# Kernel tuning notes

Measured on AMD Instinct MI355X. Metric: run time of the kernel, lower is better.

Reference implementation:

```python
import jax, jax.numpy as jnp
import numpy as np

LN_EPS = 1e-5

def split_feature(x, ns):
    # [b,h,w,c] -> [b*ns*ns, h/ns, w/ns, c] (channel_last window split)
    b, h, w, c = x.shape
    return (x.reshape(b, ns, h // ns, ns, w // ns, c)
             .transpose(0, 1, 3, 2, 4, 5)
             .reshape(b * ns * ns, h // ns, w // ns, c))

def merge_splits(x, ns):
    bn, hs, ws, c = x.shape
    b = bn // (ns * ns)
    return (x.reshape(b, ns, ns, hs, ws, c)
             .transpose(0, 1, 3, 2, 4, 5)
             .reshape(b, hs * ns, ws * ns, c))

def layer_norm(x, g, b):
    mu = jnp.mean(x, axis=-1, keepdims=True)
    var = jnp.mean(jnp.square(x - mu), axis=-1, keepdims=True)
    return (x - mu) * jax.lax.rsqrt(var + LN_EPS) * g + b

def swin_attention(q, k, v, ns, h, w, attn_mask):
    # single-head shifted-window attention, q/k/v: [b, h*w, c]
    b, _, c = q.shape
    q = q.reshape(b, h, w, c)
    k = k.reshape(b, h, w, c)
    v = v.reshape(b, h, w, c)
    sh, sw = (h // ns) // 2, (w // ns) // 2
    q = jnp.roll(q, (-sh, -sw), axis=(1, 2))
    k = jnp.roll(k, (-sh, -sw), axis=(1, 2))
    v = jnp.roll(v, (-sh, -sw), axis=(1, 2))
    qw = split_feature(q, ns).reshape(b * ns * ns, -1, c)
    kw = split_feature(k, ns).reshape(b * ns * ns, -1, c)
    vw = split_feature(v, ns).reshape(b * ns * ns, -1, c)
    scale = 1.0 / jnp.sqrt(jnp.asarray(c, qw.dtype))
    scores = jnp.einsum('blc,bsc->bls', qw, kw) * scale
    scores = scores + jnp.tile(attn_mask, (b, 1, 1))  # mask: [ns*ns, Lw, Lw]
    attn = jax.nn.softmax(scores, axis=-1)
    out = jnp.einsum('bls,bsc->blc', attn, vw)
    out = merge_splits(out.reshape(b * ns * ns, h // ns, w // ns, c), ns)
    out = jnp.roll(out, (sh, sw), axis=(1, 2))
    return out.reshape(b, h * w, c)

def transformer_layer(source, target, mask, Wq, Wk, Wv, Wm,
                      ln1_g, ln1_b, W1, W2, ln2_g, ln2_b, h, w, ns):
    q = source @ Wq.T
    k = target @ Wk.T
    v = target @ Wv.T
    msg = swin_attention(q, k, v, ns, h, w, mask)
    msg = layer_norm(msg @ Wm.T, ln1_g, ln1_b)
    hid = jnp.concatenate([source, msg], axis=-1) @ W1.T
    msg = jax.nn.gelu(hid, approximate=False) @ W2.T
    msg = layer_norm(msg, ln2_g, ln2_b)
    return source + msg

def setup_inputs() -> dict:
    key = jax.random.key(0)
    ks = jax.random.split(key, 12)
    b, h, w, d = 8, 64, 64, 256
    ns = 2
    Lw = (h // ns) * (w // ns)
    s = 0.02
    return {
        'source': jax.random.normal(ks[0], (b, h * w, d), jnp.float32),
        'target': jax.random.normal(ks[1], (b, h * w, d), jnp.float32),
        'shifted_window_attn_mask': jax.random.normal(ks[2], (ns * ns, Lw, Lw), jnp.float32),
        'Wq': jax.random.normal(ks[3], (d, d), jnp.float32) * s,
        'Wk': jax.random.normal(ks[4], (d, d), jnp.float32) * s,
        'Wv': jax.random.normal(ks[5], (d, d), jnp.float32) * s,
        'Wm': jax.random.normal(ks[6], (d, d), jnp.float32) * s,
        'ln1_g': jnp.ones((d,), jnp.float32),
        'ln1_b': jnp.zeros((d,), jnp.float32),
        'W1': jax.random.normal(ks[7], (2 * d * 4, 2 * d), jnp.float32) * s,
        'W2': jax.random.normal(ks[8], (d, 2 * d * 4), jnp.float32) * s,
        'ln2_g': jnp.ones((d,), jnp.float32),
        'ln2_b': jnp.zeros((d,), jnp.float32),
        'height': h,
        'width': w,
        'attn_num_splits': ns,
    }

def reference(source, target, shifted_window_attn_mask, Wq, Wk, Wv, Wm,
              ln1_g, ln1_b, W1, W2, ln2_g, ln2_b, height, width, attn_num_splits):
    return transformer_layer(source, target, shifted_window_attn_mask,
                             Wq, Wk, Wv, Wm, ln1_g, ln1_b, W1, W2,
                             ln2_g, ln2_b, height, width, attn_num_splits)
```

## Files before the change

### kernel.cpp

```cpp
#include <hip/hip_runtime.h>
#include <hip/hip_bf16.h>


using bf16 = __hip_bfloat16;
typedef __attribute__((ext_vector_type(8))) short short8;
typedef __attribute__((ext_vector_type(4))) float f32x4;

__device__ __forceinline__ float bf2f(unsigned short b) {
    return __uint_as_float(((unsigned)b) << 16);
}
__device__ __forceinline__ unsigned short f2bf(float f) {
    unsigned u = __float_as_uint(f);
    unsigned r = (u + 0x7FFFu + ((u >> 16) & 1u)) >> 16;
    return (unsigned short)r;
}
__device__ __forceinline__ void cp16(const void* g, void* l) {
    __builtin_amdgcn_global_load_lds((const __attribute__((address_space(1))) void*)g,
                                     (__attribute__((address_space(3))) void*)l,
                                     16, 0, 0);
}
__device__ __forceinline__ float fast_gelu(float v) {
    const float z = v * (0.7978845608028654f + 0.0356774081f * v * v);
    const float t = 1.f - 2.f / (__expf(2.f * z) + 1.f);
    return 0.5f * v * (1.f + t);
}

constexpr int MODE_PLAIN = 0;
constexpr int MODE_QKV   = 1;
constexpr int MODE_GELU  = 3;

template<int MODE, bool CONCAT>
__global__ __launch_bounds__(256)
void gemm_bt(const bf16* __restrict__ A, const bf16* __restrict__ A2,
             const bf16* __restrict__ Bm, void* __restrict__ C,
             int K, int ldc, long sAz, long sBz, int nlog)
{
    __shared__ __align__(16) bf16 As[128 * 64];
    __shared__ __align__(16) bf16 Bs[128 * 64];

    const int z = blockIdx.z;
    A  += (long)z * sAz;
    Bm += (long)z * sBz;

    const int tid  = threadIdx.x;
    const int wave = tid >> 6, lane = tid & 63;
    const int wm = wave >> 1, wn = wave & 1;
    const int quad = lane >> 4, lrow = lane & 15;

    int m0, n0;
    if (nlog >= 0) {
        const int lin = blockIdx.x;
        const int xcd = lin & 7;
        const int s   = lin >> 3;
        const int ni  = s & ((1 << nlog) - 1);
        const int mi  = ((s >> nlog) << 3) | xcd;
        m0 = mi * 128; n0 = ni * 128;
    } else {
        m0 = blockIdx.x * 128; n0 = blockIdx.y * 128;
    }

    f32x4 acc[4][4];
#pragma unroll
    for (int i = 0; i < 4; i++)
#pragma unroll
        for (int j = 0; j < 4; j++) acc[i][j] = (f32x4){0.f, 0.f, 0.f, 0.f};

    for (int k0 = 0; k0 < K; k0 += 64) {
#pragma unroll
        for (int i = 0; i < 4; ++i) {
            const int li  = i * 256 + tid;
            const int row = li >> 3, g = li & 7;
            const int sgo = ((g ^ row) & 7) << 3;
            const bf16* ga;
            if (CONCAT) {
                ga = (k0 < 256) ? (A  + (long)(m0 + row) * 256 + k0 + sgo)
                                : (A2 + (long)(m0 + row) * 256 + (k0 - 256) + sgo);
            } else {
                ga = A + (long)(m0 + row) * K + k0 + sgo;
            }
            cp16(ga, As + (li << 3));
            const bf16* gb = Bm + (long)(n0 + row) * K + k0 + sgo;
            cp16(gb, Bs + (li << 3));
        }
        __syncthreads();

#pragma unroll
        for (int s = 0; s < 2; ++s) {
            short8 af[4], bfv[4];
#pragma unroll
            for (int i = 0; i < 4; i++) {
                const int ra = wm * 64 + i * 16 + lrow;
                const int rb = wn * 64 + i * 16 + lrow;
                const int h  = (s << 2) + quad;
                af[i]  = *(const short8*)(As + ra * 64 + (((h ^ ra) & 7) << 3));
                bfv[i] = *(const short8*)(Bs + rb * 64 + (((h ^ rb) & 7) << 3));
            }
#pragma unroll
            for (int i = 0; i < 4; i++)
#pragma unroll
                for (int j = 0; j < 4; j++)
                    acc[i][j] = __builtin_amdgcn_mfma_f32_16x16x32_bf16(
                        af[i], bfv[j], acc[i][j], 0, 0, 0);
        }
        __syncthreads();
    }

    unsigned short* outb = (unsigned short*)C;
    if (MODE == MODE_QKV) {
#pragma unroll
        for (int i = 0; i < 4; i++)
#pragma unroll
            for (int j = 0; j < 4; j++)
#pragma unroll
                for (int r = 0; r < 4; r++) {
                    const int gm = m0 + wm * 64 + i * 16 + quad * 4 + r;
                    const int gn = n0 + wn * 64 + j * 16 + lrow;
                    const int batch = gm >> 12, pos = gm & 4095;
                    const int ii = pos >> 6, jj = pos & 63;
                    const int ri = (ii + 48) & 63, rj = (jj + 48) & 63;
                    const long prow =
                        ((long)((batch << 2) + ((ri >> 5) << 1) + (rj >> 5)) << 10)
                        + ((ri & 31) << 5) + (rj & 31);
                    outb[prow * 256 + gn] = f2bf(acc[i][j][r]);
                }
    } else {
#pragma unroll
        for (int i = 0; i < 4; i++)
#pragma unroll
            for (int j = 0; j < 4; j++)
#pragma unroll
                for (int r = 0; r < 4; r++) {
                    const int gm = m0 + wm * 64 + i * 16 + quad * 4 + r;
                    const int gn = n0 + wn * 64 + j * 16 + lrow;
                    float v = acc[i][j][r];
                    if (MODE == MODE_GELU) v = fast_gelu(v);
                    outb[(long)gm * ldc + gn] = f2bf(v);
                }
    }
}

__device__ __forceinline__ void stage_kv(const bf16* __restrict__ Kp,
                                         const bf16* __restrict__ Vp,
                                         bf16* ksl, bf16* vsl,
                                         int kb0, int tid)
{
#pragma unroll
    for (int i = 0; i < 4; ++i) {
        const int li = i * 256 + tid;
        const int key = li >> 5, g = li & 31;
        const int sg = (g & 24) | ((g ^ key) & 7);
        cp16(Kp + (long)(kb0 + key) * 256 + (sg << 3), ksl + (li << 3));
    }
#pragma unroll
    for (int i = 0; i < 4; ++i) {
        const int li = i * 256 + tid;
        const int ch = li >> 2, g = li & 3;
        cp16(Vp + ((long)ch << 10) + kb0 + (g << 3), vsl + (li << 3));
    }
}

__global__ __launch_bounds__(256)
void flash_attn(const bf16* __restrict__ Q, const bf16* __restrict__ Kw,
                const bf16* __restrict__ VT, const bf16* __restrict__ mask16,
                bf16* __restrict__ msg)
{
    __shared__ __align__(16) bf16 Ks[2 * 32 * 256];
    __shared__ __align__(16) bf16 Vs[2 * 256 * 32];
    __shared__ __align__(16) unsigned short Pm[4][16 * 32];

    const int f   = blockIdx.x;
    const int win = (f & 7) | ((f >> 7) << 3);
    const int qb  = (f >> 3) & 15;
    const int m0  = qb << 6;

    const bf16* Qp = Q  + ((long)win << 18);
    const bf16* Kp = Kw + ((long)win << 18);
    const bf16* Vp = VT + ((long)win << 18);
    const unsigned short* mk =
        (const unsigned short*)mask16 + ((long)(win & 3) << 20);

    const int tid = threadIdx.x;
    const int wave = tid >> 6, lane = tid & 63;
    const int quad = lane >> 4, lrow = lane & 15;
    unsigned short* Pw = Pm[wave];

    short8 qf[8];
    {
        const bf16* qr = Qp + (long)(m0 + (wave << 4) + lrow) * 256 + quad * 8;
#pragma unroll
        for (int kc = 0; kc < 8; ++kc) qf[kc] = *(const short8*)(qr + kc * 32);
    }

    f32x4 o[16];
#pragma unroll
    for (int nf = 0; nf < 16; ++nf) o[nf] = (f32x4){0.f, 0.f, 0.f, 0.f};
    float l_lane[4] = {0.f, 0.f, 0.f, 0.f};

    stage_kv(Kp, Vp, Ks, Vs, 0, tid);

    const int mrow = m0 + (wave << 4) + (quad << 2);

    for (int kt = 0; kt < 32; ++kt) {
        const int cur = kt & 1;
        const int kb0 = kt << 5;

        unsigned short mreg[2][4];
#pragma unroll
        for (int r = 0; r < 4; ++r)
#pragma unroll
            for (int nf = 0; nf < 2; ++nf)
                mreg[nf][r] = mk[((long)(mrow + r) << 10)
                                 | (kb0 + (nf << 4) + lrow)];

        const int nxt = ((kt + 1) & 31) << 5;
        stage_kv(Kp, Vp, Ks + (cur ^ 1) * 8192, Vs + (cur ^ 1) * 8192, nxt, tid);

        asm volatile("s_waitcnt vmcnt(16)" ::: "memory");
        __builtin_amdgcn_sched_barrier(0);
        __builtin_amdgcn_s_barrier();
        __builtin_amdgcn_sched_barrier(0);

        f32x4 s[2];
        s[0] = (f32x4){0.f, 0.f, 0.f, 0.f};
        s[1] = (f32x4){0.f, 0.f, 0.f, 0.f};
        const bf16* kbase = Ks + cur * 8192;
        __builtin_amdgcn_s_setprio(1);
#pragma unroll
        for (int nf = 0; nf < 2; ++nf) {
            const int key = (nf << 4) + lrow;
            short8 kb[8];
#pragma unroll
            for (int kc = 0; kc < 8; ++kc) {
                const int g = (kc << 2) + quad;
                const int sg = (g & 24) | ((g ^ key) & 7);
                kb[kc] = *(const short8*)(kbase + (key << 8) + (sg << 3));
            }
#pragma unroll
            for (int kc = 0; kc < 8; ++kc)
                s[nf] = __builtin_amdgcn_mfma_f32_16x16x32_bf16(
                    qf[kc], kb[kc], s[nf], 0, 0, 0);
        }
        __builtin_amdgcn_s_setprio(0);

#pragma unroll
        for (int r = 0; r < 4; ++r) {
            const int prow = (quad << 2) + r;
#pragma unroll
            for (int nf = 0; nf < 2; ++nf) {
                const float e = __expf(s[nf][r] * 0.0625f + bf2f(mreg[nf][r]));
                l_lane[r] += e;
                Pw[(prow << 5) + (nf << 4) + lrow] = f2bf(e);
            }
        }
        asm volatile("s_waitcnt lgkmcnt(0)" ::: "memory");
        __builtin_amdgcn_sched_barrier(0);

        const short8 af = *(const short8*)((const unsigned short*)Pw
                                           + (lrow << 5) + (quad << 3));
        const bf16* vbase = Vs + cur * 8192;
        __builtin_amdgcn_s_setprio(1);
#pragma unroll
        for (int nf = 0; nf < 16; ++nf) {
            const int vc = (nf << 4) + lrow;
            const short8 bfv = *(const short8*)(vbase + (vc << 5) + (quad << 3));
            o[nf] = __builtin_amdgcn_mfma_f32_16x16x32_bf16(af, bfv, o[nf], 0, 0, 0);
        }
        __builtin_amdgcn_s_setprio(0);

        __builtin_amdgcn_sched_barrier(0);
        __builtin_amdgcn_s_barrier();
        __builtin_amdgcn_sched_barrier(0);
    }

    float l[4];
#pragma unroll
    for (int r = 0; r < 4; ++r) {
        float v = l_lane[r];
#pragma unroll
        for (int off = 1; off < 16; off <<= 1) v += __shfl_xor(v, off, 64);
        l[r] = v;
    }
    const int batch = win >> 2;
    const int s1 = (win >> 1) & 1, s2 = win & 1;
    unsigned short* outb = (unsigned short*)msg;
#pragma unroll
    for (int r = 0; r < 4; ++r) {
        const float inv = 1.f / l[r];
        const int gm = m0 + (wave << 4) + (quad << 2) + r;
        const int r5 = gm >> 5, c5 = gm & 31;
        const int ii = ((s1 << 5) + r5 + 16) & 63;
        const int jj = ((s2 << 5) + c5 + 16) & 63;
        const long mr = (long)batch * 4096 + ii * 64 + jj;
#pragma unroll
        for (int nf = 0; nf < 16; ++nf) {
            const int gn = (nf << 4) + lrow;
            outb[mr * 256 + gn] = f2bf(o[nf][r] * inv);
        }
    }
}

__global__ __launch_bounds__(256)
void cvtw_k(const float* __restrict__ w0, const float* __restrict__ w1,
            const float* __restrict__ w2, const float* __restrict__ w3,
            const float* __restrict__ w4, const float* __restrict__ w5,
            const float* __restrict__ w6, unsigned short* __restrict__ d)
{
    const float* s; long n4, off4;
    switch (blockIdx.y) {
    case 0:  s = w0; n4 = 16384;   off4 = 0;      break;
    case 1:  s = w1; n4 = 16384;   off4 = 16384;  break;
    case 2:  s = w2; n4 = 16384;   off4 = 32768;  break;
    case 3:  s = w3; n4 = 16384;   off4 = 49152;  break;
    case 4:  s = w4; n4 = 262144;  off4 = 65536;  break;
    case 5:  s = w5; n4 = 131072;  off4 = 327680; break;
    default: s = w6; n4 = 1048576; off4 = 458752; break;
    }
    ushort4* dst = (ushort4*)d + off4;
    for (long i = (long)blockIdx.x * 256 + threadIdx.x; i < n4;
         i += (long)gridDim.x * 256) {
        const float4 v = ((const float4*)s)[i];
        ushort4 o;
        o.x = f2bf(v.x); o.y = f2bf(v.y); o.z = f2bf(v.z); o.w = f2bf(v.w);
        dst[i] = o;
    }
}

__global__ __launch_bounds__(256)
void cvt_k(const float* __restrict__ s, unsigned short* __restrict__ d, long n4)
{
    for (long i = (long)blockIdx.x * 256 + threadIdx.x; i < n4;
         i += (long)gridDim.x * 256) {
        const float4 v = ((const float4*)s)[i];
        ushort4 o;
        o.x = f2bf(v.x); o.y = f2bf(v.y); o.z = f2bf(v.z); o.w = f2bf(v.w);
        ((ushort4*)d)[i] = o;
    }
}

__global__ __launch_bounds__(256)
void transpose_vw(const bf16* __restrict__ vw, bf16* __restrict__ vwT)
{
    __shared__ bf16 t[64][65];
    const int win = blockIdx.z;
    const int s0 = blockIdx.x * 64, c0 = blockIdx.y * 64;
    const bf16* src = vw  + ((long)win << 18);
    bf16*       dst = vwT + ((long)win << 18);
    const int tid = threadIdx.x;
#pragma unroll
    for (int ii = 0; ii < 16; ++ii) {
        const int lin = ii * 256 + tid;
        const int r = lin >> 6, c = lin & 63;
        t[r][c] = src[(long)(s0 + r) * 256 + c0 + c];
    }
    __syncthreads();
#pragma unroll
    for (int ii = 0; ii < 16; ++ii) {
        const int lin = ii * 256 + tid;
        const int r = lin >> 6, c = lin & 63;
        dst[(long)(c0 + r) * 1024 + s0 + c] = t[c][r];
    }
}

__global__ __launch_bounds__(256)
void ln1_k(const bf16* __restrict__ x, const float* __restrict__ g,
           const float* __restrict__ be, bf16* __restrict__ out)
{
    const int wave = threadIdx.x >> 6, lane = threadIdx.x & 63;
    const long row = (long)blockIdx.x * 4 + wave;
    const ushort4 u = ((const ushort4*)((const unsigned short*)x + (row << 8)))[lane];
    const float v0 = bf2f(u.x), v1 = bf2f(u.y), v2 = bf2f(u.z), v3 = bf2f(u.w);
    float s = v0 + v1 + v2 + v3;
    float q = v0 * v0 + v1 * v1 + v2 * v2 + v3 * v3;
#pragma unroll
    for (int o = 1; o < 64; o <<= 1) { s += __shfl_xor(s, o, 64); q += __shfl_xor(q, o, 64); }
    const float mean = s * 0.00390625f;
    const float var  = q * 0.00390625f - mean * mean;
    const float inv  = rsqrtf(fmaxf(var, 0.f) + 1e-5f);
    const float4 gg = ((const float4*)g)[lane];
    const float4 bb = ((const float4*)be)[lane];
    ushort4 o4;
    o4.x = f2bf((v0 - mean) * inv * gg.x + bb.x);
    o4.y = f2bf((v1 - mean) * inv * gg.y + bb.y);
    o4.z = f2bf((v2 - mean) * inv * gg.z + bb.z);
    o4.w = f2bf((v3 - mean) * inv * gg.w + bb.w);
    ((ushort4*)((unsigned short*)out + (row << 8)))[lane] = o4;
}

__global__ __launch_bounds__(256)
void ln2_k(const bf16* __restrict__ x, const float* __restrict__ g,
           const float* __restrict__ be, const float* __restrict__ res,
           float* __restrict__ out)
{
    const int wave = threadIdx.x >> 6, lane = threadIdx.x & 63;
    const long row = (long)blockIdx.x * 4 + wave;
    const ushort4 u = ((const ushort4*)((const unsigned short*)x + (row << 8)))[lane];
    const float v0 = bf2f(u.x), v1 = bf2f(u.y), v2 = bf2f(u.z), v3 = bf2f(u.w);
    float s = v0 + v1 + v2 + v3;
    float q = v0 * v0 + v1 * v1 + v2 * v2 + v3 * v3;
#pragma unroll
    for (int o = 1; o < 64; o <<= 1) { s += __shfl_xor(s, o, 64); q += __shfl_xor(q, o, 64); }
    const float mean = s * 0.00390625f;
    const float var  = q * 0.00390625f - mean * mean;
    const float inv  = rsqrtf(fmaxf(var, 0.f) + 1e-5f);
    const float4 gg = ((const float4*)g)[lane];
    const float4 bb = ((const float4*)be)[lane];
    const float4 rr = ((const float4*)(res + (row << 8)))[lane];
    float4 o4;
    o4.x = (v0 - mean) * inv * gg.x + bb.x + rr.x;
    o4.y = (v1 - mean) * inv * gg.y + bb.y + rr.y;
    o4.z = (v2 - mean) * inv * gg.z + bb.z + rr.z;
    o4.w = (v3 - mean) * inv * gg.w + bb.w + rr.w;
    ((float4*)(out + (row << 8)))[lane] = o4;
}

extern "C" void kernel_launch(void* const* d_in, const int* in_sizes, int n_in,
                              void* d_out, int out_size, void* d_ws, size_t ws_size,
                              hipStream_t stream)
{
    const float* source = (const float*)d_in[0];
    const float* target = (const float*)d_in[1];
    const float* mask   = (const float*)d_in[2];
    const float* Wq = (const float*)d_in[3];
    const float* Wk = (const float*)d_in[4];
    const float* Wv = (const float*)d_in[5];
    const float* Wm = (const float*)d_in[6];
    const float* ln1g = (const float*)d_in[7];
    const float* ln1b = (const float*)d_in[8];
    const float* W1 = (const float*)d_in[9];
    const float* W2 = (const float*)d_in[10];
    const float* ln2g = (const float*)d_in[11];
    const float* ln2b = (const float*)d_in[12];
    float* out = (float*)d_out;

    char* ws = (char*)d_ws;
    const size_t MB = 1ull << 20;

    bf16* RA = (bf16*)(ws +  0 * MB);
    bf16* RB = (bf16*)(ws + 16 * MB);
    bf16* RC = (bf16*)(ws + 32 * MB);
    unsigned short* D = (unsigned short*)(ws + 48 * MB);
    bf16* Wq16 = (bf16*)(D);
    bf16* Wk16 = (bf16*)(D + 65536);
    bf16* Wv16 = (bf16*)(D + 131072);
    bf16* Wm16 = (bf16*)(D + 196608);
    bf16* W116 = (bf16*)(D + 262144);
    bf16* W216 = (bf16*)(D + 1310720);
    bf16* mask16 = (bf16*)(D + 1835008);
    bf16* tgt16 = (bf16*)d_out;
    bf16* src16 = (bf16*)((char*)d_out + 16777216);
    bf16* msgb  = (bf16*)d_out;

    const bool bigws = ws_size >= (200ull << 20);
    bf16* hidbig = (bf16*)(ws + 64 * MB);

    cvtw_k<<<dim3(256, 7), 256, 0, stream>>>(Wq, Wk, Wv, Wm, W1, W2, mask, D);
    cvt_k<<<4096, 256, 0, stream>>>(target, (unsigned short*)tgt16, 2097152);
    cvt_k<<<4096, 256, 0, stream>>>(source, (unsigned short*)src16, 2097152);

    gemm_bt<MODE_QKV, false><<<dim3(512, 1, 1), 256, 0, stream>>>(
        tgt16, nullptr, Wv16, RB, 256, 256, 0, 0, 1);
    transpose_vw<<<dim3(16, 4, 32), 256, 0, stream>>>(RB, RC);
    gemm_bt<MODE_QKV, false><<<dim3(512, 1, 1), 256, 0, stream>>>(
        tgt16, nullptr, Wk16, RB, 256, 256, 0, 0, 1);
    gemm_bt<MODE_QKV, false><<<dim3(512, 1, 1), 256, 0, stream>>>(
        src16, nullptr, Wq16, RA, 256, 256, 0, 0, 1);

    flash_attn<<<dim3(512), 256, 0, stream>>>(RA, RB, RC, mask16, msgb);

    gemm_bt<MODE_PLAIN, false><<<dim3(512, 1, 1), 256, 0, stream>>>(
        msgb, nullptr, Wm16, RB, 256, 256, 0, 0, 1);
    ln1_k<<<8192, 256, 0, stream>>>(RB, ln1g, ln1b, RC);

    if (bigws) {
        gemm_bt<MODE_GELU, true><<<dim3(4096, 1, 1), 256, 0, stream>>>(
            src16, RC, W116, hidbig, 512, 2048, 0, 0, 4);
        gemm_bt<MODE_PLAIN, false><<<dim3(512, 1, 1), 256, 0, stream>>>(
            hidbig, nullptr, W216, RB, 2048, 256, 0, 0, 1);
    } else {
        bf16* hid = (bf16*)d_out;
        cvt_k<<<8192, 256, 0, stream>>>(source, (unsigned short*)RA, 2097152);
        for (int sl = 0; sl < 4; ++sl) {
            const long ro = (long)sl * 8192 * 256;
            gemm_bt<MODE_GELU, true><<<dim3(64, 16, 1), 256, 0, stream>>>(
                RA + ro, RC + ro, W116, hid, 512, 2048, 0, 0, -1);
            gemm_bt<MODE_PLAIN, false><<<dim3(64, 2, 1), 256, 0, stream>>>(
                hid, nullptr, W216, RB + ro, 2048, 256, 0, 0, -1);
        }
    }

    ln2_k<<<8192, 256, 0, stream>>>(RB, ln2g, ln2b, source, out);
}
```

Baseline: 444.7 us.

## Double-buffer GEMM LDS tiles with async prefetch of next K slice

```diff
diff --git a/kernel.cpp b/kernel.cpp
--- a/kernel.cpp
+++ b/kernel.cpp
@@ -35,8 +35,8 @@
              const bf16* __restrict__ Bm, void* __restrict__ C,
              int K, int ldc, long sAz, long sBz, int nlog)
 {
-    __shared__ __align__(16) bf16 As[128 * 64];
-    __shared__ __align__(16) bf16 Bs[128 * 64];
+    __shared__ __align__(16) bf16 As[2][128 * 64];
+    __shared__ __align__(16) bf16 Bs[2][128 * 64];
 
     const int z = blockIdx.z;
     A  += (long)z * sAz;
@@ -59,41 +59,66 @@
         m0 = blockIdx.x * 128; n0 = blockIdx.y * 128;
     }
 
+    int srow[4], sgo[4], lofs[4];
+#pragma unroll
+    for (int i = 0; i < 4; ++i) {
+        const int li = i * 256 + tid;
+        srow[i] = li >> 3;
+        sgo[i]  = (((li & 7) ^ srow[i]) & 7) << 3;
+        lofs[i] = li << 3;
+    }
+
     f32x4 acc[4][4];
 #pragma unroll
     for (int i = 0; i < 4; i++)
 #pragma unroll
         for (int j = 0; j < 4; j++) acc[i][j] = (f32x4){0.f, 0.f, 0.f, 0.f};
 
+#define STAGE_TILE(b, k0s)                                                     \
+    do {                                                                       \
+        _Pragma("unroll")                                                      \
+        for (int i = 0; i < 4; ++i) {                                          \
+            const bf16* ga;                                                    \
+            if (CONCAT) {                                                      \
+                ga = ((k0s) < 256)                                             \
+                   ? (A  + (long)(m0 + srow[i]) * 256 + (k0s) + sgo[i])        \
+                   : (A2 + (long)(m0 + srow[i]) * 256 + ((k0s) - 256) + sgo[i]);\
+            } else {                                                           \
+                ga = A + (long)(m0 + srow[i]) * K + (k0s) + sgo[i];            \
+            }                                                                  \
+            cp16(ga, &As[b][lofs[i]]);                                         \
+            const bf16* gb = Bm + (long)(n0 + srow[i]) * K + (k0s) + sgo[i];   \
+            cp16(gb, &Bs[b][lofs[i]]);                                         \
+        }                                                                      \
+    } while (0)
+
+    STAGE_TILE(0, 0);
+    __builtin_amdgcn_sched_barrier(0);
+
+    int buf = 0;
     for (int k0 = 0; k0 < K; k0 += 64) {
-#pragma unroll
-        for (int i = 0; i < 4; ++i) {
-            const int li  = i * 256 + tid;
-            const int row = li >> 3, g = li & 7;
-            const int sgo = ((g ^ row) & 7) << 3;
-            const bf16* ga;
-            if (CONCAT) {
-                ga = (k0 < 256) ? (A  + (long)(m0 + row) * 256 + k0 + sgo)
-                                : (A2 + (long)(m0 + row) * 256 + (k0 - 256) + sgo);
-            } else {
-                ga = A + (long)(m0 + row) * K + k0 + sgo;
-            }
-            cp16(ga, As + (li << 3));
-            const bf16* gb = Bm + (long)(n0 + row) * K + k0 + sgo;
-            cp16(gb, Bs + (li << 3));
-        }
-        __syncthreads();
-
-#pragma unroll
-        for (int s = 0; s < 2; ++s) {
+        const int nxt = (k0 + 64 < K) ? (k0 + 64) : 0;
+        STAGE_TILE(buf ^ 1, nxt);
+        __builtin_amdgcn_sched_barrier(0);
+
+        asm volatile("s_waitcnt vmcnt(8)" ::: "memory");
+        __builtin_amdgcn_sched_barrier(0);
+        __builtin_amdgcn_s_barrier();
+        __builtin_amdgcn_sched_barrier(0);
+
+        const bf16* Ab = As[buf];
+        const bf16* Bb = Bs[buf];
+        __builtin_amdgcn_s_setprio(1);
+#pragma unroll
+        for (int sl = 0; sl < 2; ++sl) {
             short8 af[4], bfv[4];
 #pragma unroll
             for (int i = 0; i < 4; i++) {
                 const int ra = wm * 64 + i * 16 + lrow;
                 const int rb = wn * 64 + i * 16 + lrow;
-                const int h  = (s << 2) + quad;
-                af[i]  = *(const short8*)(As + ra * 64 + (((h ^ ra) & 7) << 3));
-                bfv[i] = *(const short8*)(Bs + rb * 64 + (((h ^ rb) & 7) << 3));
+                const int h  = (sl << 2) + quad;
+                af[i]  = *(const short8*)(Ab + ra * 64 + (((h ^ ra) & 7) << 3));
+                bfv[i] = *(const short8*)(Bb + rb * 64 + (((h ^ rb) & 7) << 3));
             }
 #pragma unroll
             for (int i = 0; i < 4; i++)
@@ -102,8 +127,14 @@
                     acc[i][j] = __builtin_amdgcn_mfma_f32_16x16x32_bf16(
                         af[i], bfv[j], acc[i][j], 0, 0, 0);
         }
-        __syncthreads();
-    }
+        __builtin_amdgcn_s_setprio(0);
+
+        __builtin_amdgcn_sched_barrier(0);
+        __builtin_amdgcn_s_barrier();
+        __builtin_amdgcn_sched_barrier(0);
+        buf ^= 1;
+    }
+#undef STAGE_TILE
 
     unsigned short* outb = (unsigned short*)C;
     if (MODE == MODE_QKV) {
```

Result: no change. 449.8 us (+1.1%).
